# Kernel tuning notes

Measured on AMD Instinct MI355X. Metric: run time of the kernel, lower is better.

## Reference

```python
import jax, jax.numpy as jnp
import numpy as np

SHIFT = 1  # original module picks random(+1/-1) at init; fixed to +1 for determinism


def setup_inputs() -> dict:
    key = jax.random.key(0)
    k1, k2, k3 = jax.random.split(key, 3)
    x = jax.random.normal(k1, (1024, 1792, 14), dtype=jnp.float32)
    w1 = jax.random.normal(k2, (256, 2), dtype=jnp.float32)      # weights[0]
    w2 = jax.random.normal(k3, (128, 3, 256), dtype=jnp.float32)  # weights[1]
    return {"x": x, "w1": w1, "w2": w2}


def reference(x, w1, w2):
    m = 1024
    # Channels 1792 split as j(128) * l(14); H = 14. unfold((3,1), pad=(1,0)) is an
    # im2col over H with 3 taps; torch orders the unfolded channel dim as c*3+k,
    # so reshape (1024, 128, 14, 3, 14) puts taps k before spatial n -> permute to mjlnk.
    x4 = x.reshape(m, 128, 14, 14)                       # (m, j, l, h)
    xp = jnp.pad(x4, ((0, 0), (0, 0), (0, 0), (1, 1)))   # pad H by 1 each side
    win = jnp.stack([xp[..., 0:14], xp[..., 1:15], xp[..., 2:16]], axis=-1)  # (m,j,l,n,k)
    t4 = jnp.einsum('mjlnk,jki->mlni', win, w2)          # (1024, 14, 14, 256)
    t5 = jnp.einsum('mabj,ji->mabji', t4, w1)            # (1024, 14, 14, 256, 2) outer product
    t6 = jnp.roll(t5, SHIFT, axis=1)
    t6 = t6.transpose(0, 2, 3, 1, 4).reshape(m, 14, 256, 28)
    t6 = jnp.roll(t6, SHIFT, axis=3)
    t6 = t6.reshape(m, 14, 256, 14, 2).sum(axis=4)       # pairwise sum
    return t6.transpose(0, 2, 3, 1)                      # (1024, 256, 14, 14)
```

## Files before the change

### kernel.cpp

```cpp
#include <hip/hip_runtime.h>
#include <hip/hip_bf16.h>

typedef __bf16 bf16x8 __attribute__((ext_vector_type(8)));
typedef unsigned short u16x8 __attribute__((ext_vector_type(8)));
typedef float f32x4 __attribute__((ext_vector_type(4)));

__device__ __forceinline__ unsigned short f2bf(float f) {
    unsigned u = __builtin_bit_cast(unsigned, f);
    u += 0x7FFFu + ((u >> 16) & 1u);
    return (unsigned short)(u >> 16);
}
__device__ __forceinline__ float bf2f(unsigned short h) {
    unsigned u = ((unsigned)h) << 16;
    return __builtin_bit_cast(float, u);
}

__global__ void prep_w2(const float* __restrict__ w2, unsigned short* __restrict__ w2t) {
    int idx = blockIdx.x * 256 + threadIdx.x;
    if (idx < 128 * 3 * 256) {
        int i  = idx % 256;
        int jk = idx / 256;
        int j2 = jk / 3, k = jk % 3;
        w2t[i * 384 + k * 128 + j2] = f2bf(w2[idx]);
    }
}

__global__ __launch_bounds__(256, 2) void fused_conv_outer(
    const float* __restrict__ x, const float* __restrict__ w1,
    const unsigned short* __restrict__ w2t, float* __restrict__ out)
{
    __shared__ alignas(16) unsigned short xlds[196 * 136];
    __shared__ alignas(16) unsigned short cb[4 * 16 * 210];

    const int m    = blockIdx.x;
    const int tid  = threadIdx.x;
    const int wave = tid >> 6;
    const int lane = tid & 63;
    const int c16  = lane & 15;
    const int kgrp = lane >> 4;

    {
        const float* xm = x + (size_t)m * 25088;
        const int j2a = 2 * lane;
        const int rbase = wave * 48;
        const int rend  = (wave == 3) ? 52 : 48;
        for (int rr = 0; rr < rend; rr += 4) {
            const float4 v0 = *(const float4*)(xm + (size_t)j2a * 196 + rbase + rr);
            const float4 v1 = *(const float4*)(xm + (size_t)(j2a + 1) * 196 + rbase + rr);
            const float a0[4] = {v0.x, v0.y, v0.z, v0.w};
            const float a1[4] = {v1.x, v1.y, v1.z, v1.w};
#pragma unroll
            for (int i2 = 0; i2 < 4; ++i2) {
                unsigned pk = (unsigned)f2bf(a0[i2]) | ((unsigned)f2bf(a1[i2]) << 16);
                *(unsigned*)&xlds[(rbase + rr + i2) * 136 + j2a] = pk;
            }
        }
    }
    __syncthreads();

    unsigned short* cbw = &cb[wave * (16 * 210)];

#pragma unroll 1
    for (int nt = 0; nt < 4; ++nt) {
        const int ntile = wave * 4 + nt;
        const int col   = ntile * 16 + c16;

        bf16x8 Bf[12];
        {
            const unsigned short* bp = w2t + (size_t)col * 384 + kgrp * 8;
#pragma unroll
            for (int k = 0; k < 12; ++k)
                Bf[k] = __builtin_bit_cast(bf16x8, *(const u16x8*)(bp + k * 32));
        }

#pragma unroll 1
        for (int mt = 0; mt < 13; ++mt) {
            const int r0 = mt * 16 + c16;
            const int rc = (r0 < 196) ? r0 : 195;
            const int nn = rc % 14;

            bf16x8 Af[12];
#pragma unroll
            for (int k = 0; k < 12; ++k) {
                const int tap = k >> 2;
                const int h   = nn + tap - 1;
                if ((unsigned)h < 14u) {
                    Af[k] = __builtin_bit_cast(bf16x8,
                        *(const u16x8*)&xlds[(rc + tap - 1) * 136 + (k & 3) * 32 + kgrp * 8]);
                } else {
                    Af[k] = __builtin_bit_cast(bf16x8, (u16x8)(unsigned short)0);
                }
            }

            f32x4 acc = {0.f, 0.f, 0.f, 0.f};
#pragma unroll
            for (int k = 0; k < 12; ++k)
                acc = __builtin_amdgcn_mfma_f32_16x16x32_bf16(Af[k], Bf[k], acc, 0, 0, 0);

            const int rr0 = mt * 16 + kgrp * 4;
            if (rr0 < 196) {
                unsigned pk0 = (unsigned)f2bf(acc[0]) | ((unsigned)f2bf(acc[1]) << 16);
                unsigned pk1 = (unsigned)f2bf(acc[2]) | ((unsigned)f2bf(acc[3]) << 16);
                *(unsigned*)&cbw[c16 * 210 + rr0]     = pk0;
                *(unsigned*)&cbw[c16 * 210 + rr0 + 2] = pk1;
            }
        }

        int r1a[4], r2a[4], ea[4]; bool oka[4];
#pragma unroll
        for (int it = 0; it < 4; ++it) {
            int e = it * 64 + lane;
            oka[it] = (e < 196);
            int ec  = oka[it] ? e : 195;
            int cdx = ec / 14;
            int nn2 = ec - cdx * 14;
            r1a[it] = ((cdx + 13) % 14) * 14 + nn2;
            r2a[it] = ((cdx + 12) % 14) * 14 + nn2;
            ea[it]  = e;
        }
        float* outb = out + (size_t)m * 50176 + (size_t)ntile * 16 * 196;
#pragma unroll
        for (int c = 0; c < 16; ++c) {
            const float2 wv = *(const float2*)(w1 + (ntile * 16 + c) * 2);
            const unsigned short* cr = cbw + c * 210;
            float* op = outb + c * 196;
#pragma unroll
            for (int it = 0; it < 4; ++it) {
                if (oka[it]) {
                    float v = wv.x * bf2f(cr[r1a[it]]) + wv.y * bf2f(cr[r2a[it]]);
                    op[ea[it]] = v;
                }
            }
        }
    }
}

extern "C" void kernel_launch(void* const* d_in, const int* in_sizes, int n_in,
                              void* d_out, int out_size, void* d_ws, size_t ws_size,
                              hipStream_t stream) {
    const float* x  = (const float*)d_in[0];
    const float* w1 = (const float*)d_in[1];
    const float* w2 = (const float*)d_in[2];
    float* out = (float*)d_out;
    unsigned short* w2t = (unsigned short*)d_ws;

    prep_w2<<<384, 256, 0, stream>>>(w2, w2t);
    fused_conv_outer<<<1024, 256, 0, stream>>>(x, w1, w2t, out);
}
```

Measured before the change: 354.1 us.

## Fold w1 and the rolls into a doubled-K GEMM with 32x32 MFMA

Folds the w1 outer-product scale into pre-scaled weight copies. The two rolled row gathers become two accumulation phases over the GEMM, so the epilogue reduces to a plain coalesced float4 store through a small fp32 LDS staging buffer. It also moves from 16x16x32 to 32x32x16 MFMA tiles with multiple M-tiles per wave sharing B loads, and drops the bf16 rounding of the intermediate. It doubles the MFMA work and weight reads, and register pressure from the large accumulators may limit occupancy.

```diff
diff --git a/kernel.cpp b/kernel.cpp
--- a/kernel.cpp
+++ b/kernel.cpp
@@ -1,43 +1,139 @@
 #include <hip/hip_runtime.h>
-#include <hip/hip_bf16.h>
 
 typedef __bf16 bf16x8 __attribute__((ext_vector_type(8)));
 typedef unsigned short u16x8 __attribute__((ext_vector_type(8)));
 typedef float f32x4 __attribute__((ext_vector_type(4)));
+typedef float f32x16 __attribute__((ext_vector_type(16)));
 
 __device__ __forceinline__ unsigned short f2bf(float f) {
     unsigned u = __builtin_bit_cast(unsigned, f);
     u += 0x7FFFu + ((u >> 16) & 1u);
     return (unsigned short)(u >> 16);
 }
-__device__ __forceinline__ float bf2f(unsigned short h) {
-    unsigned u = ((unsigned)h) << 16;
-    return __builtin_bit_cast(float, u);
-}
 
-__global__ void prep_w2(const float* __restrict__ w2, unsigned short* __restrict__ w2t) {
+__global__ void prep_w(const float* __restrict__ w1, const float* __restrict__ w2,
+                       unsigned short* __restrict__ wt) {
     int idx = blockIdx.x * 256 + threadIdx.x;
     if (idx < 128 * 3 * 256) {
-        int i  = idx % 256;
-        int jk = idx / 256;
-        int j2 = jk / 3, k = jk % 3;
-        w2t[i * 384 + k * 128 + j2] = f2bf(w2[idx]);
+        int i  = idx & 255;
+        int jk = idx >> 8;
+        int j2 = jk / 3, k = jk - 3 * j2;
+        float v = w2[idx];
+        wt[(size_t)i * 768 + k * 128 + j2]       = f2bf(w1[2 * i] * v);
+        wt[(size_t)i * 768 + 384 + k * 128 + j2] = f2bf(w1[2 * i + 1] * v);
     }
 }
 
-__global__ __launch_bounds__(256, 2) void fused_conv_outer(
-    const float* __restrict__ x, const float* __restrict__ w1,
-    const unsigned short* __restrict__ w2t, float* __restrict__ out)
+
+#define XSTRIDE 136
+#define CBSTR   36
+
+template<int NM>
+__device__ __forceinline__ void gemm_group(
+    int mt0, const unsigned short* xl, const unsigned short* wt,
+    float* cbw, float* outm, int wave, int lane)
 {
-    __shared__ alignas(16) unsigned short xlds[196 * 136];
-    __shared__ alignas(16) unsigned short cb[4 * 16 * 210];
+    const int l32 = lane & 31, half = lane >> 5;
+    const int c0 = wave * 64 + l32;
+
+    int rb1[NM][3], rb2[NM][3];
+#pragma unroll
+    for (int mi = 0; mi < NM; ++mi) {
+        int e  = (mt0 + mi) * 32 + l32;
+        int ec = e < 196 ? e : 195;
+        int cdx = ec / 14;
+        int n   = ec - 14 * cdx;
+        int lA = (cdx + 13) % 14;
+        int lB = (cdx + 12) % 14;
+#pragma unroll
+        for (int t = 0; t < 3; ++t) {
+            bool valid = (t == 1) || ((t == 0) ? (n >= 1) : (n <= 12));
+            int rA = valid ? (lA * 14 + n + t - 1) : 196;
+            int rB = valid ? (lB * 14 + n + t - 1) : 196;
+            rb1[mi][t] = rA * XSTRIDE + half * 8;
+            rb2[mi][t] = rB * XSTRIDE + half * 8;
+        }
+    }
+
+    f32x16 acc[NM][2];
+#pragma unroll
+    for (int mi = 0; mi < NM; ++mi)
+#pragma unroll
+        for (int nt = 0; nt < 2; ++nt)
+#pragma unroll
+            for (int q = 0; q < 16; ++q) acc[mi][nt][q] = 0.f;
+
+    const unsigned short* wb0 = wt + (size_t)c0 * 768 + half * 8;
+
+#pragma unroll 1
+    for (int ph = 0; ph < 2; ++ph) {
+        int rbp[NM][3];
+#pragma unroll
+        for (int mi = 0; mi < NM; ++mi)
+#pragma unroll
+            for (int t = 0; t < 3; ++t)
+                rbp[mi][t] = (ph == 0) ? rb1[mi][t] : rb2[mi][t];
+        const unsigned short* wb = wb0 + ph * 384;
+#pragma unroll
+        for (int tap = 0; tap < 3; ++tap) {
+#pragma unroll
+            for (int ss = 0; ss < 8; ++ss) {
+                const int ko = tap * 128 + ss * 16;
+                u16x8 b0 = *(const u16x8*)(wb + ko);
+                u16x8 b1 = *(const u16x8*)(wb + 32 * 768 + ko);
+#pragma unroll
+                for (int mi = 0; mi < NM; ++mi) {
+                    u16x8 av = *(const u16x8*)(xl + rbp[mi][tap] + ss * 16);
+                    acc[mi][0] = __builtin_amdgcn_mfma_f32_32x32x16_bf16(
+                        __builtin_bit_cast(bf16x8, av), __builtin_bit_cast(bf16x8, b0),
+                        acc[mi][0], 0, 0, 0);
+                    acc[mi][1] = __builtin_amdgcn_mfma_f32_32x32x16_bf16(
+                        __builtin_bit_cast(bf16x8, av), __builtin_bit_cast(bf16x8, b1),
+                        acc[mi][1], 0, 0, 0);
+                }
+            }
+        }
+    }
+
+    const int ib = lane >> 3;
+    const int eo = (lane & 7) * 4;
+#pragma unroll
+    for (int mi = 0; mi < NM; ++mi) {
+        const int mt = mt0 + mi;
+#pragma unroll
+        for (int nt = 0; nt < 2; ++nt) {
+#pragma unroll
+            for (int q = 0; q < 4; ++q) {
+                f32x4 v = { acc[mi][nt][q * 4 + 0], acc[mi][nt][q * 4 + 1],
+                            acc[mi][nt][q * 4 + 2], acc[mi][nt][q * 4 + 3] };
+                *(f32x4*)&cbw[l32 * CBSTR + q * 8 + half * 4] = v;
+            }
+            asm volatile("s_waitcnt lgkmcnt(0)" ::: "memory");
+#pragma unroll
+            for (int r = 0; r < 4; ++r) {
+                f32x4 v = *(const f32x4*)&cbw[(r * 8 + ib) * CBSTR + eo];
+                if (mt < 6 || eo == 0) {
+                    float* op = outm + (size_t)(wave * 64 + nt * 32 + r * 8 + ib) * 196
+                                     + mt * 32 + eo;
+                    *(f32x4*)op = v;
+                }
+            }
+            asm volatile("s_waitcnt lgkmcnt(0)" ::: "memory");
+        }
+    }
+}
+
+__global__ __launch_bounds__(256, 2) void fused_conv_outer2(
+    const float* __restrict__ x, const unsigned short* __restrict__ wt,
+    float* __restrict__ out)
+{
+    __shared__ alignas(16) unsigned short xlds[197 * XSTRIDE];
+    __shared__ alignas(16) float cb[4][32 * CBSTR];
 
     const int m    = blockIdx.x;
     const int tid  = threadIdx.x;
     const int wave = tid >> 6;
     const int lane = tid & 63;
-    const int c16  = lane & 15;
-    const int kgrp = lane >> 4;
 
     {
         const float* xm = x + (size_t)m * 25088;
@@ -52,87 +148,17 @@
 #pragma unroll
             for (int i2 = 0; i2 < 4; ++i2) {
                 unsigned pk = (unsigned)f2bf(a0[i2]) | ((unsigned)f2bf(a1[i2]) << 16);
-                *(unsigned*)&xlds[(rbase + rr + i2) * 136 + j2a] = pk;
+                *(unsigned*)&xlds[(rbase + rr + i2) * XSTRIDE + j2a] = pk;
             }
         }
+        if (tid < XSTRIDE / 2)
+            ((unsigned*)&xlds[196 * XSTRIDE])[tid] = 0u;
     }
     __syncthreads();
 
-    unsigned short* cbw = &cb[wave * (16 * 210)];
-
-#pragma unroll 1
-    for (int nt = 0; nt < 4; ++nt) {
-        const int ntile = wave * 4 + nt;
-        const int col   = ntile * 16 + c16;
-
-        bf16x8 Bf[12];
-        {
-            const unsigned short* bp = w2t + (size_t)col * 384 + kgrp * 8;
-#pragma unroll
-            for (int k = 0; k < 12; ++k)
-                Bf[k] = __builtin_bit_cast(bf16x8, *(const u16x8*)(bp + k * 32));
-        }
-
-#pragma unroll 1
-        for (int mt = 0; mt < 13; ++mt) {
-            const int r0 = mt * 16 + c16;
-            const int rc = (r0 < 196) ? r0 : 195;
-            const int nn = rc % 14;
-
-            bf16x8 Af[12];
-#pragma unroll
-            for (int k = 0; k < 12; ++k) {
-                const int tap = k >> 2;
-                const int h   = nn + tap - 1;
-                if ((unsigned)h < 14u) {
-                    Af[k] = __builtin_bit_cast(bf16x8,
-                        *(const u16x8*)&xlds[(rc + tap - 1) * 136 + (k & 3) * 32 + kgrp * 8]);
-                } else {
-                    Af[k] = __builtin_bit_cast(bf16x8, (u16x8)(unsigned short)0);
-                }
-            }
-
-            f32x4 acc = {0.f, 0.f, 0.f, 0.f};
-#pragma unroll
-            for (int k = 0; k < 12; ++k)
-                acc = __builtin_amdgcn_mfma_f32_16x16x32_bf16(Af[k], Bf[k], acc, 0, 0, 0);
-
-            const int rr0 = mt * 16 + kgrp * 4;
-            if (rr0 < 196) {
-                unsigned pk0 = (unsigned)f2bf(acc[0]) | ((unsigned)f2bf(acc[1]) << 16);
-                unsigned pk1 = (unsigned)f2bf(acc[2]) | ((unsigned)f2bf(acc[3]) << 16);
-                *(unsigned*)&cbw[c16 * 210 + rr0]     = pk0;
-                *(unsigned*)&cbw[c16 * 210 + rr0 + 2] = pk1;
-            }
-        }
-
-        int r1a[4], r2a[4], ea[4]; bool oka[4];
-#pragma unroll
-        for (int it = 0; it < 4; ++it) {
-            int e = it * 64 + lane;
-            oka[it] = (e < 196);
-            int ec  = oka[it] ? e : 195;
-            int cdx = ec / 14;
-            int nn2 = ec - cdx * 14;
-            r1a[it] = ((cdx + 13) % 14) * 14 + nn2;
-            r2a[it] = ((cdx + 12) % 14) * 14 + nn2;
-            ea[it]  = e;
-        }
-        float* outb = out + (size_t)m * 50176 + (size_t)ntile * 16 * 196;
-#pragma unroll
-        for (int c = 0; c < 16; ++c) {
-            const float2 wv = *(const float2*)(w1 + (ntile * 16 + c) * 2);
-            const unsigned short* cr = cbw + c * 210;
-            float* op = outb + c * 196;
-#pragma unroll
-            for (int it = 0; it < 4; ++it) {
-                if (oka[it]) {
-                    float v = wv.x * bf2f(cr[r1a[it]]) + wv.y * bf2f(cr[r2a[it]]);
-                    op[ea[it]] = v;
-                }
-            }
-        }
-    }
+    float* outm = out + (size_t)m * 50176;
+    gemm_group<4>(0, xlds, wt, cb[wave], outm, wave, lane);
+    gemm_group<3>(4, xlds, wt, cb[wave], outm, wave, lane);
 }
 
 extern "C" void kernel_launch(void* const* d_in, const int* in_sizes, int n_in,
@@ -142,8 +168,8 @@
     const float* w1 = (const float*)d_in[1];
     const float* w2 = (const float*)d_in[2];
     float* out = (float*)d_out;
-    unsigned short* w2t = (unsigned short*)d_ws;
+    unsigned short* wt = (unsigned short*)d_ws;
 
-    prep_w2<<<384, 256, 0, stream>>>(w2, w2t);
-    fused_conv_outer<<<1024, 256, 0, stream>>>(x, w1, w2t, out);
+    prep_w<<<384, 256, 0, stream>>>(w1, w2, wt);
+    fused_conv_outer2<<<1024, 256, 0, stream>>>(x, wt, out);
 }
```

New measurement: 423.7 us. +19.7%, slower.
